# Kernel tuning notes

Hardware: AMD Instinct MI355X
Metric: run time of the kernel (lower is better)

## Reference

```python
import jax, jax.numpy as jnp
from jax import lax
import numpy as np

KSIZE = 21

def setup_inputs() -> dict:
    key = jax.random.key(0)
    k1, k2 = jax.random.split(key)
    x = jax.random.normal(k1, (32, 3, 512, 512), dtype=jnp.float32)
    kernel = jax.random.uniform(k2, (32, 1, KSIZE, KSIZE), dtype=jnp.float32)
    return {"x": x, "kernel": kernel}

def reference(x, kernel):
    # Per-sample depthwise conv: fuse batch loop into a single grouped conv
    # by folding batch into channels (groups = B*C).
    B, C, H, W = x.shape
    K = kernel.shape[-1]
    pad = K // 2
    # expand the per-sample kernel across channels, shape (B*C, 1, K, K)
    k = jnp.broadcast_to(kernel, (B, C, K, K)).reshape(B * C, 1, K, K)
    xr = x.reshape(1, B * C, H, W)
    out = lax.conv_general_dilated(
        xr, k,
        window_strides=(1, 1),
        padding=[(pad, pad), (pad, pad)],
        dimension_numbers=("NCHW", "OIHW", "NCHW"),
        feature_group_count=B * C,
    )
    return out.reshape(B, C, H, W)
```

## Files before the change

### kernel.cpp

```cpp
#include <hip/hip_runtime.h>

#define KK 21
#define HH 512
#define WW 512
#define CC 3
#define BB 32
#define TILE_Y 64
#define TILE_X 128
#define SROWS 85
#define SSTRIDE 168
#define NKHP 11
#define NB_PER_B (NKHP * 3 * 512)
#define NCHUNK 20

typedef __attribute__((ext_vector_type(8))) short short8;
typedef __attribute__((ext_vector_type(4))) float floatx4;

__device__ __forceinline__ unsigned short f2bf(float f) {
    union { float f; unsigned u; } v; v.f = f;
    unsigned r = v.u + 0x7FFF + ((v.u >> 16) & 1);
    return (unsigned short)(r >> 16);
}

__global__ __launch_bounds__(256) void build_B(
    const float* __restrict__ ker, unsigned short* __restrict__ wsB)
{
    const int b = blockIdx.x;
    const float* __restrict__ kp = ker + b * KK * KK;
    unsigned short* __restrict__ wb = wsB + (size_t)b * NB_PER_B;
    for (int e = threadIdx.x; e < NB_PER_B; e += 256) {
        const int j    = e & 7;
        const int n    = (e >> 3) & 15;
        const int q    = (e >> 7) & 3;
        const int f    = e >> 9;
        const int khp  = f / 3;
        const int half = f - khp * 3;
        const int k    = q * 8 + j;
        const int h    = k >> 4;
        const int c    = k & 15;
        const int kh   = 2 * khp + h;
        const int d    = c - n - 2 + 16 * half;
        float v = 0.0f;
        if (kh < KK && d >= 0 && d < KK) v = kp[kh * KK + d];
        wb[e] = f2bf(v);
    }
}

__global__ __launch_bounds__(256, 4) void dwconv_mfma(
    const float* __restrict__ x,
    const unsigned short* __restrict__ wsB,
    float* __restrict__ out)
{
    __shared__ __align__(16) unsigned short s_in[SROWS * SSTRIDE];

    const int tiles = (HH / TILE_Y) * (WW / TILE_X);
    const int bc = blockIdx.x / tiles;
    const int t  = blockIdx.x % tiles;
    const int ty0 = (t / (WW / TILE_X)) * TILE_Y;
    const int tx0 = (t % (WW / TILE_X)) * TILE_X;
    const int b = bc / CC;

    const float* __restrict__ xp = x + (size_t)bc * HH * WW;
    const unsigned short* __restrict__ wsb = wsB + (size_t)b * NB_PER_B;
    const int tid = threadIdx.x;

    for (int i = tid; i < SROWS * NCHUNK; i += 256) {
        const int ly  = i / NCHUNK;
        const int k   = i - ly * NCHUNK;
        const int gy  = ty0 - 10 + ly;
        const int gx0 = tx0 - 12 + 8 * k;
        float4 v0 = make_float4(0.f, 0.f, 0.f, 0.f);
        float4 v1 = make_float4(0.f, 0.f, 0.f, 0.f);
        if (gy >= 0 && gy < HH) {
            const float* __restrict__ rp = xp + (size_t)gy * WW;
            if (gx0 >= 0 && gx0 + 7 < WW) {
                v0 = *(const float4*)(rp + gx0);
                v1 = *(const float4*)(rp + gx0 + 4);
            } else {
                if (gx0 + 0 >= 0 && gx0 + 0 < WW) v0.x = rp[gx0 + 0];
                if (gx0 + 1 >= 0 && gx0 + 1 < WW) v0.y = rp[gx0 + 1];
                if (gx0 + 2 >= 0 && gx0 + 2 < WW) v0.z = rp[gx0 + 2];
                if (gx0 + 3 >= 0 && gx0 + 3 < WW) v0.w = rp[gx0 + 3];
                if (gx0 + 4 >= 0 && gx0 + 4 < WW) v1.x = rp[gx0 + 4];
                if (gx0 + 5 >= 0 && gx0 + 5 < WW) v1.y = rp[gx0 + 5];
                if (gx0 + 6 >= 0 && gx0 + 6 < WW) v1.z = rp[gx0 + 6];
                if (gx0 + 7 >= 0 && gx0 + 7 < WW) v1.w = rp[gx0 + 7];
            }
        }
        const int p0 = (int)((unsigned)f2bf(v0.x) | ((unsigned)f2bf(v0.y) << 16));
        const int p1 = (int)((unsigned)f2bf(v0.z) | ((unsigned)f2bf(v0.w) << 16));
        const int p2 = (int)((unsigned)f2bf(v1.x) | ((unsigned)f2bf(v1.y) << 16));
        const int p3 = (int)((unsigned)f2bf(v1.z) | ((unsigned)f2bf(v1.w) << 16));
        *(int4*)&s_in[ly * SSTRIDE + 8 * k] = make_int4(p0, p1, p2, p3);
    }
    __syncthreads();

    const int lane = tid & 63;
    const int wv   = tid >> 6;
    const int mrow = lane & 15;
    const int qd   = lane >> 4;

    floatx4 acc[8];
#pragma unroll
    for (int tt = 0; tt < 8; ++tt) acc[tt] = (floatx4){0.f, 0.f, 0.f, 0.f};

    const unsigned short* bbase = wsb + lane * 8;
    const unsigned short* abase = s_in + ((16 * wv + mrow + (qd >> 1)) * SSTRIDE) + 8 * (qd & 1);

    short8 nb1 = *(const short8*)(bbase);
    short8 nb2 = *(const short8*)(bbase + 512);
    short8 nb3 = *(const short8*)(bbase + 1024);

#pragma unroll 1
    for (int khp = 0; khp < NKHP; ++khp) {
        const short8 b1 = nb1;
        const short8 b2 = nb2;
        const short8 b3 = nb3;
        const int khn = (khp < NKHP - 1) ? (khp + 1) : khp;
        nb1 = *(const short8*)(bbase + khn * 1536);
        nb2 = *(const short8*)(bbase + khn * 1536 + 512);
        nb3 = *(const short8*)(bbase + khn * 1536 + 1024);

        const unsigned short* arow = abase + 2 * khp * SSTRIDE;
        short8 a[10];
#pragma unroll
        for (int s = 0; s < 10; ++s) a[s] = *(const short8*)(arow + 16 * s);

#pragma unroll
        for (int tt = 0; tt < 8; ++tt) {
            acc[tt] = __builtin_amdgcn_mfma_f32_16x16x32_bf16(a[tt],     b1, acc[tt], 0, 0, 0);
            acc[tt] = __builtin_amdgcn_mfma_f32_16x16x32_bf16(a[tt + 1], b2, acc[tt], 0, 0, 0);
            acc[tt] = __builtin_amdgcn_mfma_f32_16x16x32_bf16(a[tt + 2], b3, acc[tt], 0, 0, 0);
        }
    }

    float* __restrict__ op = out + (size_t)bc * HH * WW;
#pragma unroll
    for (int tt = 0; tt < 8; ++tt) {
#pragma unroll
        for (int r = 0; r < 4; ++r) {
            const int y = ty0 + 16 * wv + qd * 4 + r;
            const int xcol = tx0 + 16 * tt + mrow;
            op[(size_t)y * WW + xcol] = acc[tt][r];
        }
    }
}

extern "C" void kernel_launch(void* const* d_in, const int* in_sizes, int n_in,
                              void* d_out, int out_size, void* d_ws, size_t ws_size,
                              hipStream_t stream) {
    const float* x   = (const float*)d_in[0];
    const float* ker = (const float*)d_in[1];
    float* out = (float*)d_out;
    unsigned short* wsB = (unsigned short*)d_ws;

    build_B<<<BB, 256, 0, stream>>>(ker, wsB);

    const int tiles = (HH / TILE_Y) * (WW / TILE_X);
    const int nblocks = BB * CC * tiles;
    dwconv_mfma<<<nblocks, 256, 0, stream>>>(x, wsB, out);
}
```

Measured before the change: 217.9 us.

## Make each block loop over row-strip tiles, prefetching the next tile into registers

Each block now handles a full 64-row strip across four horizontal tiles. While the MFMA loop computes the current tile, global loads for the next tile are issued into registers, then converted to bf16 and written to LDS after a barrier. This is meant to hide global-load latency behind compute. The block index is also remapped across the grid, and occupancy drops to 3 blocks per SM because the 56 staging registers per thread raise register pressure. The trade-off is fewer blocks, giving less parallelism for tail balancing, plus two extra barriers per tile.

```diff
diff --git a/kernel.cpp b/kernel.cpp
--- a/kernel.cpp
+++ b/kernel.cpp
@@ -12,6 +12,9 @@
 #define NKHP 11
 #define NB_PER_B (NKHP * 3 * 512)
 #define NCHUNK 20
+#define NSTG (SROWS * NCHUNK)
+#define NT 4
+#define NBLK (BB * CC * (HH / TILE_Y))
 
 typedef __attribute__((ext_vector_type(8))) short short8;
 typedef __attribute__((ext_vector_type(4))) float floatx4;
@@ -46,25 +49,14 @@
     }
 }
 
-__global__ __launch_bounds__(256, 4) void dwconv_mfma(
-    const float* __restrict__ x,
-    const unsigned short* __restrict__ wsB,
-    float* __restrict__ out)
-{
-    __shared__ __align__(16) unsigned short s_in[SROWS * SSTRIDE];
-
-    const int tiles = (HH / TILE_Y) * (WW / TILE_X);
-    const int bc = blockIdx.x / tiles;
-    const int t  = blockIdx.x % tiles;
-    const int ty0 = (t / (WW / TILE_X)) * TILE_Y;
-    const int tx0 = (t % (WW / TILE_X)) * TILE_X;
-    const int b = bc / CC;
-
-    const float* __restrict__ xp = x + (size_t)bc * HH * WW;
-    const unsigned short* __restrict__ wsb = wsB + (size_t)b * NB_PER_B;
-    const int tid = threadIdx.x;
-
-    for (int i = tid; i < SROWS * NCHUNK; i += 256) {
+__device__ __forceinline__ void load_stage(
+    const float* __restrict__ xp, int ty0, int tx0, int tid,
+    float4 (&sv0)[7], float4 (&sv1)[7])
+{
+#pragma unroll
+    for (int it = 0; it < 7; ++it) {
+        const int i = tid + 256 * it;
+        if (it == 6 && i >= NSTG) continue;
         const int ly  = i / NCHUNK;
         const int k   = i - ly * NCHUNK;
         const int gy  = ty0 - 10 + ly;
@@ -87,61 +79,111 @@
                 if (gx0 + 7 >= 0 && gx0 + 7 < WW) v1.w = rp[gx0 + 7];
             }
         }
-        const int p0 = (int)((unsigned)f2bf(v0.x) | ((unsigned)f2bf(v0.y) << 16));
-        const int p1 = (int)((unsigned)f2bf(v0.z) | ((unsigned)f2bf(v0.w) << 16));
-        const int p2 = (int)((unsigned)f2bf(v1.x) | ((unsigned)f2bf(v1.y) << 16));
-        const int p3 = (int)((unsigned)f2bf(v1.z) | ((unsigned)f2bf(v1.w) << 16));
+        sv0[it] = v0;
+        sv1[it] = v1;
+    }
+}
+
+__device__ __forceinline__ void cvt_write(
+    unsigned short* __restrict__ s_in, int tid,
+    const float4 (&sv0)[7], const float4 (&sv1)[7])
+{
+#pragma unroll
+    for (int it = 0; it < 7; ++it) {
+        const int i = tid + 256 * it;
+        if (it == 6 && i >= NSTG) continue;
+        const int ly = i / NCHUNK;
+        const int k  = i - ly * NCHUNK;
+        const int p0 = (int)((unsigned)f2bf(sv0[it].x) | ((unsigned)f2bf(sv0[it].y) << 16));
+        const int p1 = (int)((unsigned)f2bf(sv0[it].z) | ((unsigned)f2bf(sv0[it].w) << 16));
+        const int p2 = (int)((unsigned)f2bf(sv1[it].x) | ((unsigned)f2bf(sv1[it].y) << 16));
+        const int p3 = (int)((unsigned)f2bf(sv1[it].z) | ((unsigned)f2bf(sv1[it].w) << 16));
         *(int4*)&s_in[ly * SSTRIDE + 8 * k] = make_int4(p0, p1, p2, p3);
     }
-    __syncthreads();
+}
+
+__global__ __launch_bounds__(256, 3) void dwconv_mfma(
+    const float* __restrict__ x,
+    const unsigned short* __restrict__ wsB,
+    float* __restrict__ out)
+{
+    __shared__ __align__(16) unsigned short s_in[SROWS * SSTRIDE];
+
+    const int rbid = (blockIdx.x & 7) * (NBLK / 8) + (blockIdx.x >> 3);
+    const int bc   = rbid >> 3;
+    const int ty0  = (rbid & 7) * TILE_Y;
+    const int b    = bc / CC;
+
+    const float* __restrict__ xp = x + (size_t)bc * HH * WW;
+    float* __restrict__ op = out + (size_t)bc * HH * WW;
+    const unsigned short* __restrict__ wsb = wsB + (size_t)b * NB_PER_B;
+    const int tid = threadIdx.x;
 
     const int lane = tid & 63;
     const int wv   = tid >> 6;
     const int mrow = lane & 15;
     const int qd   = lane >> 4;
 
-    floatx4 acc[8];
-#pragma unroll
-    for (int tt = 0; tt < 8; ++tt) acc[tt] = (floatx4){0.f, 0.f, 0.f, 0.f};
-
     const unsigned short* bbase = wsb + lane * 8;
     const unsigned short* abase = s_in + ((16 * wv + mrow + (qd >> 1)) * SSTRIDE) + 8 * (qd & 1);
 
-    short8 nb1 = *(const short8*)(bbase);
-    short8 nb2 = *(const short8*)(bbase + 512);
-    short8 nb3 = *(const short8*)(bbase + 1024);
+    float4 sv0[7], sv1[7];
+
+    load_stage(xp, ty0, 0, tid, sv0, sv1);
+    cvt_write(s_in, tid, sv0, sv1);
+    __syncthreads();
+
+    for (int t0 = 0; t0 < NT; ++t0) {
+        const int tx0 = t0 * TILE_X;
+
+        if (t0 + 1 < NT)
+            load_stage(xp, ty0, tx0 + TILE_X, tid, sv0, sv1);
+
+        floatx4 acc[8];
+#pragma unroll
+        for (int tt = 0; tt < 8; ++tt) acc[tt] = (floatx4){0.f, 0.f, 0.f, 0.f};
+
+        short8 nb1 = *(const short8*)(bbase);
+        short8 nb2 = *(const short8*)(bbase + 512);
+        short8 nb3 = *(const short8*)(bbase + 1024);
 
 #pragma unroll 1
-    for (int khp = 0; khp < NKHP; ++khp) {
-        const short8 b1 = nb1;
-        const short8 b2 = nb2;
-        const short8 b3 = nb3;
-        const int khn = (khp < NKHP - 1) ? (khp + 1) : khp;
-        nb1 = *(const short8*)(bbase + khn * 1536);
-        nb2 = *(const short8*)(bbase + khn * 1536 + 512);
-        nb3 = *(const short8*)(bbase + khn * 1536 + 1024);
-
-        const unsigned short* arow = abase + 2 * khp * SSTRIDE;
-        short8 a[10];
-#pragma unroll
-        for (int s = 0; s < 10; ++s) a[s] = *(const short8*)(arow + 16 * s);
+        for (int khp = 0; khp < NKHP; ++khp) {
+            const short8 b1 = nb1;
+            const short8 b2 = nb2;
+            const short8 b3 = nb3;
+            const int khn = (khp < NKHP - 1) ? (khp + 1) : khp;
+            nb1 = *(const short8*)(bbase + khn * 1536);
+            nb2 = *(const short8*)(bbase + khn * 1536 + 512);
+            nb3 = *(const short8*)(bbase + khn * 1536 + 1024);
+
+            const unsigned short* arow = abase + 2 * khp * SSTRIDE;
+            short8 a[10];
+#pragma unroll
+            for (int s = 0; s < 10; ++s) a[s] = *(const short8*)(arow + 16 * s);
+
+#pragma unroll
+            for (int tt = 0; tt < 8; ++tt) {
+                acc[tt] = __builtin_amdgcn_mfma_f32_16x16x32_bf16(a[tt],     b1, acc[tt], 0, 0, 0);
+                acc[tt] = __builtin_amdgcn_mfma_f32_16x16x32_bf16(a[tt + 1], b2, acc[tt], 0, 0, 0);
+                acc[tt] = __builtin_amdgcn_mfma_f32_16x16x32_bf16(a[tt + 2], b3, acc[tt], 0, 0, 0);
+            }
+        }
 
 #pragma unroll
         for (int tt = 0; tt < 8; ++tt) {
-            acc[tt] = __builtin_amdgcn_mfma_f32_16x16x32_bf16(a[tt],     b1, acc[tt], 0, 0, 0);
-            acc[tt] = __builtin_amdgcn_mfma_f32_16x16x32_bf16(a[tt + 1], b2, acc[tt], 0, 0, 0);
-            acc[tt] = __builtin_amdgcn_mfma_f32_16x16x32_bf16(a[tt + 2], b3, acc[tt], 0, 0, 0);
-        }
-    }
-
-    float* __restrict__ op = out + (size_t)bc * HH * WW;
-#pragma unroll
-    for (int tt = 0; tt < 8; ++tt) {
-#pragma unroll
-        for (int r = 0; r < 4; ++r) {
-            const int y = ty0 + 16 * wv + qd * 4 + r;
-            const int xcol = tx0 + 16 * tt + mrow;
-            op[(size_t)y * WW + xcol] = acc[tt][r];
+#pragma unroll
+            for (int r = 0; r < 4; ++r) {
+                const int y = ty0 + 16 * wv + qd * 4 + r;
+                const int xcol = tx0 + 16 * tt + mrow;
+                op[(size_t)y * WW + xcol] = acc[tt][r];
+            }
+        }
+
+        if (t0 + 1 < NT) {
+            __syncthreads();
+            cvt_write(s_in, tid, sv0, sv1);
+            __syncthreads();
         }
     }
 }
@@ -156,7 +198,5 @@
 
     build_B<<<BB, 256, 0, stream>>>(ker, wsB);
 
-    const int tiles = (HH / TILE_Y) * (WW / TILE_X);
-    const int nblocks = BB * CC * tiles;
-    dwconv_mfma<<<nblocks, 256, 0, stream>>>(x, wsB, out);
-}
+    dwconv_mfma<<<NBLK, 256, 0, stream>>>(x, wsB, out);
+}
```

Measured after the change: 240.6 us. 10.4% more time.

## Warp-specialize depthwise conv with double-buffered LDS producer waves over persistent tiles

Applied to the files above, without the earlier changes.

The kernel becomes a fixed grid of 512 blocks, each processing 6 tiles. Two producer waves stage the next tile's input (converted to bf16) into a second LDS buffer while four compute waves run the MFMA convolution on the current one. Block IDs are remapped so consecutive tiles are spread across XCDs. The aim is to hide global-load and conversion latency behind MFMA work. In exchange, LDS use per block doubles and there are fewer compute waves per CU, which may reduce how much latency is hidden within the MFMA loop.

```diff
diff --git a/kernel.cpp b/kernel.cpp
--- a/kernel.cpp
+++ b/kernel.cpp
@@ -12,6 +12,11 @@
 #define NKHP 11
 #define NB_PER_B (NKHP * 3 * 512)
 #define NCHUNK 20
+#define NSTG (SROWS * NCHUNK)
+#define NTHREADS 384
+#define NCOMPUTE 4
+#define TILES_PER_BLK 6
+#define NBLK 512
 
 typedef __attribute__((ext_vector_type(8))) short short8;
 typedef __attribute__((ext_vector_type(4))) float floatx4;
@@ -46,103 +51,149 @@
     }
 }
 
-__global__ __launch_bounds__(256, 4) void dwconv_mfma(
+__device__ __forceinline__ void ld_chunk(
+    const float* __restrict__ xp, int ty0, int tx0, int i,
+    float4& v0, float4& v1)
+{
+    const int ly  = i / NCHUNK;
+    const int k   = i - ly * NCHUNK;
+    const int gy  = ty0 - 10 + ly;
+    const int gx0 = tx0 - 12 + 8 * k;
+    v0 = make_float4(0.f, 0.f, 0.f, 0.f);
+    v1 = make_float4(0.f, 0.f, 0.f, 0.f);
+    if (gy >= 0 && gy < HH) {
+        const float* __restrict__ rp = xp + (size_t)gy * WW;
+        if (gx0 >= 0 && gx0 + 7 < WW) {
+            v0 = *(const float4*)(rp + gx0);
+            v1 = *(const float4*)(rp + gx0 + 4);
+        } else {
+            if (gx0 + 0 >= 0 && gx0 + 0 < WW) v0.x = rp[gx0 + 0];
+            if (gx0 + 1 >= 0 && gx0 + 1 < WW) v0.y = rp[gx0 + 1];
+            if (gx0 + 2 >= 0 && gx0 + 2 < WW) v0.z = rp[gx0 + 2];
+            if (gx0 + 3 >= 0 && gx0 + 3 < WW) v0.w = rp[gx0 + 3];
+            if (gx0 + 4 >= 0 && gx0 + 4 < WW) v1.x = rp[gx0 + 4];
+            if (gx0 + 5 >= 0 && gx0 + 5 < WW) v1.y = rp[gx0 + 5];
+            if (gx0 + 6 >= 0 && gx0 + 6 < WW) v1.z = rp[gx0 + 6];
+            if (gx0 + 7 >= 0 && gx0 + 7 < WW) v1.w = rp[gx0 + 7];
+        }
+    }
+}
+
+__device__ __forceinline__ void wr_chunk(
+    unsigned short* __restrict__ sbuf, int i,
+    const float4& v0, const float4& v1)
+{
+    const int ly = i / NCHUNK;
+    const int k  = i - ly * NCHUNK;
+    const int p0 = (int)((unsigned)f2bf(v0.x) | ((unsigned)f2bf(v0.y) << 16));
+    const int p1 = (int)((unsigned)f2bf(v0.z) | ((unsigned)f2bf(v0.w) << 16));
+    const int p2 = (int)((unsigned)f2bf(v1.x) | ((unsigned)f2bf(v1.y) << 16));
+    const int p3 = (int)((unsigned)f2bf(v1.z) | ((unsigned)f2bf(v1.w) << 16));
+    *(int4*)&sbuf[ly * SSTRIDE + 8 * k] = make_int4(p0, p1, p2, p3);
+}
+
+__device__ __forceinline__ void stage_tile(
+    const float* __restrict__ x, unsigned short* __restrict__ sbuf,
+    int t, int ptid)
+{
+    const int bc  = t >> 5;
+    const int rem = t & 31;
+    const int ty0 = (rem >> 2) * TILE_Y;
+    const int tx0 = (rem & 3) * TILE_X;
+    const float* __restrict__ xp = x + (size_t)bc * HH * WW;
+
+    for (int i0 = ptid; i0 < NSTG; i0 += 512) {
+        float4 a0, a1, b0, b1, c0, c1, d0, d1;
+        const int i1 = i0 + 128, i2 = i0 + 256, i3 = i0 + 384;
+        ld_chunk(xp, ty0, tx0, i0, a0, a1);
+        if (i1 < NSTG) ld_chunk(xp, ty0, tx0, i1, b0, b1);
+        if (i2 < NSTG) ld_chunk(xp, ty0, tx0, i2, c0, c1);
+        if (i3 < NSTG) ld_chunk(xp, ty0, tx0, i3, d0, d1);
+        wr_chunk(sbuf, i0, a0, a1);
+        if (i1 < NSTG) wr_chunk(sbuf, i1, b0, b1);
+        if (i2 < NSTG) wr_chunk(sbuf, i2, c0, c1);
+        if (i3 < NSTG) wr_chunk(sbuf, i3, d0, d1);
+    }
+}
+
+__global__ __launch_bounds__(NTHREADS, 3) void dwconv_mfma(
     const float* __restrict__ x,
     const unsigned short* __restrict__ wsB,
     float* __restrict__ out)
 {
-    __shared__ __align__(16) unsigned short s_in[SROWS * SSTRIDE];
-
-    const int tiles = (HH / TILE_Y) * (WW / TILE_X);
-    const int bc = blockIdx.x / tiles;
-    const int t  = blockIdx.x % tiles;
-    const int ty0 = (t / (WW / TILE_X)) * TILE_Y;
-    const int tx0 = (t % (WW / TILE_X)) * TILE_X;
-    const int b = bc / CC;
-
-    const float* __restrict__ xp = x + (size_t)bc * HH * WW;
-    const unsigned short* __restrict__ wsb = wsB + (size_t)b * NB_PER_B;
-    const int tid = threadIdx.x;
-
-    for (int i = tid; i < SROWS * NCHUNK; i += 256) {
-        const int ly  = i / NCHUNK;
-        const int k   = i - ly * NCHUNK;
-        const int gy  = ty0 - 10 + ly;
-        const int gx0 = tx0 - 12 + 8 * k;
-        float4 v0 = make_float4(0.f, 0.f, 0.f, 0.f);
-        float4 v1 = make_float4(0.f, 0.f, 0.f, 0.f);
-        if (gy >= 0 && gy < HH) {
-            const float* __restrict__ rp = xp + (size_t)gy * WW;
-            if (gx0 >= 0 && gx0 + 7 < WW) {
-                v0 = *(const float4*)(rp + gx0);
-                v1 = *(const float4*)(rp + gx0 + 4);
-            } else {
-                if (gx0 + 0 >= 0 && gx0 + 0 < WW) v0.x = rp[gx0 + 0];
-                if (gx0 + 1 >= 0 && gx0 + 1 < WW) v0.y = rp[gx0 + 1];
-                if (gx0 + 2 >= 0 && gx0 + 2 < WW) v0.z = rp[gx0 + 2];
-                if (gx0 + 3 >= 0 && gx0 + 3 < WW) v0.w = rp[gx0 + 3];
-                if (gx0 + 4 >= 0 && gx0 + 4 < WW) v1.x = rp[gx0 + 4];
-                if (gx0 + 5 >= 0 && gx0 + 5 < WW) v1.y = rp[gx0 + 5];
-                if (gx0 + 6 >= 0 && gx0 + 6 < WW) v1.z = rp[gx0 + 6];
-                if (gx0 + 7 >= 0 && gx0 + 7 < WW) v1.w = rp[gx0 + 7];
+    __shared__ __align__(16) unsigned short s_in[2][SROWS * SSTRIDE];
+
+    const int rbid   = (blockIdx.x & 7) * (NBLK / 8) + (blockIdx.x >> 3);
+    const int t_base = rbid * TILES_PER_BLK;
+    const int tid  = threadIdx.x;
+    const int wv   = tid >> 6;
+    const int lane = tid & 63;
+    const int mrow = lane & 15;
+    const int qd   = lane >> 4;
+    const bool producer = (wv >= NCOMPUTE);
+    const int ptid = tid - NCOMPUTE * 64;
+
+    if (producer) stage_tile(x, s_in[0], t_base, ptid);
+    __syncthreads();
+
+    for (int i = 0; i < TILES_PER_BLK; ++i) {
+        const int t = t_base + i;
+        if (producer) {
+            if (i + 1 < TILES_PER_BLK)
+                stage_tile(x, s_in[(i + 1) & 1], t + 1, ptid);
+        } else {
+            const int bc  = t >> 5;
+            const int rem = t & 31;
+            const int ty0 = (rem >> 2) * TILE_Y;
+            const int tx0 = (rem & 3) * TILE_X;
+            const int b   = bc / CC;
+            const unsigned short* __restrict__ sbuf = s_in[i & 1];
+            const unsigned short* bbase = wsB + (size_t)b * NB_PER_B + lane * 8;
+            const unsigned short* abase = sbuf + ((16 * wv + mrow + (qd >> 1)) * SSTRIDE) + 8 * (qd & 1);
+
+            floatx4 acc[8];
+#pragma unroll
+            for (int tt = 0; tt < 8; ++tt) acc[tt] = (floatx4){0.f, 0.f, 0.f, 0.f};
+
+            short8 nb1 = *(const short8*)(bbase);
+            short8 nb2 = *(const short8*)(bbase + 512);
+            short8 nb3 = *(const short8*)(bbase + 1024);
+
+#pragma unroll 1
+            for (int khp = 0; khp < NKHP; ++khp) {
+                const short8 b1 = nb1;
+                const short8 b2 = nb2;
+                const short8 b3 = nb3;
+                const int khn = (khp < NKHP - 1) ? (khp + 1) : khp;
+                nb1 = *(const short8*)(bbase + khn * 1536);
+                nb2 = *(const short8*)(bbase + khn * 1536 + 512);
+                nb3 = *(const short8*)(bbase + khn * 1536 + 1024);
+
+                const unsigned short* arow = abase + 2 * khp * SSTRIDE;
+                short8 a[10];
+#pragma unroll
+                for (int s = 0; s < 10; ++s) a[s] = *(const short8*)(arow + 16 * s);
+
+#pragma unroll
+                for (int tt = 0; tt < 8; ++tt) {
+                    acc[tt] = __builtin_amdgcn_mfma_f32_16x16x32_bf16(a[tt],     b1, acc[tt], 0, 0, 0);
+                    acc[tt] = __builtin_amdgcn_mfma_f32_16x16x32_bf16(a[tt + 1], b2, acc[tt], 0, 0, 0);
+                    acc[tt] = __builtin_amdgcn_mfma_f32_16x16x32_bf16(a[tt + 2], b3, acc[tt], 0, 0, 0);
+                }
+            }
+
+            float* __restrict__ op = out + (size_t)bc * HH * WW;
+#pragma unroll
+            for (int tt = 0; tt < 8; ++tt) {
+#pragma unroll
+                for (int r = 0; r < 4; ++r) {
+                    const int y = ty0 + 16 * wv + qd * 4 + r;
+                    const int xcol = tx0 + 16 * tt + mrow;
+                    op[(size_t)y * WW + xcol] = acc[tt][r];
+                }
             }
         }
-        const int p0 = (int)((unsigned)f2bf(v0.x) | ((unsigned)f2bf(v0.y) << 16));
-        const int p1 = (int)((unsigned)f2bf(v0.z) | ((unsigned)f2bf(v0.w) << 16));
-        const int p2 = (int)((unsigned)f2bf(v1.x) | ((unsigned)f2bf(v1.y) << 16));
-        const int p3 = (int)((unsigned)f2bf(v1.z) | ((unsigned)f2bf(v1.w) << 16));
-        *(int4*)&s_in[ly * SSTRIDE + 8 * k] = make_int4(p0, p1, p2, p3);
-    }
-    __syncthreads();
-
-    const int lane = tid & 63;
-    const int wv   = tid >> 6;
-    const int mrow = lane & 15;
-    const int qd   = lane >> 4;
-
-    floatx4 acc[8];
-#pragma unroll
-    for (int tt = 0; tt < 8; ++tt) acc[tt] = (floatx4){0.f, 0.f, 0.f, 0.f};
-
-    const unsigned short* bbase = wsb + lane * 8;
-    const unsigned short* abase = s_in + ((16 * wv + mrow + (qd >> 1)) * SSTRIDE) + 8 * (qd & 1);
-
-    short8 nb1 = *(const short8*)(bbase);
-    short8 nb2 = *(const short8*)(bbase + 512);
-    short8 nb3 = *(const short8*)(bbase + 1024);
-
-#pragma unroll 1
-    for (int khp = 0; khp < NKHP; ++khp) {
-        const short8 b1 = nb1;
-        const short8 b2 = nb2;
-        const short8 b3 = nb3;
-        const int khn = (khp < NKHP - 1) ? (khp + 1) : khp;
-        nb1 = *(const short8*)(bbase + khn * 1536);
-        nb2 = *(const short8*)(bbase + khn * 1536 + 512);
-        nb3 = *(const short8*)(bbase + khn * 1536 + 1024);
-
-        const unsigned short* arow = abase + 2 * khp * SSTRIDE;
-        short8 a[10];
-#pragma unroll
-        for (int s = 0; s < 10; ++s) a[s] = *(const short8*)(arow + 16 * s);
-
-#pragma unroll
-        for (int tt = 0; tt < 8; ++tt) {
-            acc[tt] = __builtin_amdgcn_mfma_f32_16x16x32_bf16(a[tt],     b1, acc[tt], 0, 0, 0);
-            acc[tt] = __builtin_amdgcn_mfma_f32_16x16x32_bf16(a[tt + 1], b2, acc[tt], 0, 0, 0);
-            acc[tt] = __builtin_amdgcn_mfma_f32_16x16x32_bf16(a[tt + 2], b3, acc[tt], 0, 0, 0);
-        }
-    }
-
-    float* __restrict__ op = out + (size_t)bc * HH * WW;
-#pragma unroll
-    for (int tt = 0; tt < 8; ++tt) {
-#pragma unroll
-        for (int r = 0; r < 4; ++r) {
-            const int y = ty0 + 16 * wv + qd * 4 + r;
-            const int xcol = tx0 + 16 * tt + mrow;
-            op[(size_t)y * WW + xcol] = acc[tt][r];
-        }
+        __syncthreads();
     }
 }
 
@@ -156,7 +207,5 @@
 
     build_B<<<BB, 256, 0, stream>>>(ker, wsB);
 
-    const int tiles = (HH / TILE_Y) * (WW / TILE_X);
-    const int nblocks = BB * CC * tiles;
-    dwconv_mfma<<<nblocks, 256, 0, stream>>>(x, wsB, out);
-}
+    dwconv_mfma<<<NBLK, NTHREADS, 0, stream>>>(x, wsB, out);
+}
```

Measured after the change: 303.7 us. +39.4%, slower.
